# Optimization experiments

Measured on AMD Instinct MI355X. Metric: run time of the kernel, lower is better.

The kernel has to match this reference:

```python
import jax, jax.numpy as jnp
import numpy as np

WS = 8            # window size (square)
HEADS = 16
HEAD_DIM = 32
DIM = 512
NEG_INF = float('-inf')


def _create_mask(ws, disp, upper_lower, left_right):
    size = ws * ws
    m = np.zeros((size, size), dtype=np.float32)
    d = disp
    if upper_lower:
        m[-d * ws:, :-d * ws] = NEG_INF
        m[:-d * ws, -d * ws:] = NEG_INF
    if left_right:
        m = m.reshape(ws, ws, ws, ws)
        m[:, -d:, :, :-d] = NEG_INF
        m[:, :-d, :, -d:] = NEG_INF
        m = m.reshape(size, size)
    return m


def _relative_indices(ws):
    coords = np.array([[x, y] for x in range(ws) for y in range(ws)])  # [ws^2, 2]
    dist = coords[None, :, :] - coords[:, None, :]                      # [ws^2, ws^2, 2]
    dist += ws - 1
    return dist.astype(np.int64)


_REL_IDX = _relative_indices(WS)                      # [64, 64, 2]
_UL_MASK = jnp.asarray(_create_mask(WS, WS // 2, True, False))   # [64, 64]
_LR_MASK = jnp.asarray(_create_mask(WS, WS // 2, False, True))   # [64, 64]


def setup_inputs() -> dict:
    key = jax.random.key(0)
    ks = jax.random.split(key, 5)
    b, n = 16, 64
    return {
        'x': jax.random.normal(ks[0], (b, n, n, DIM), dtype=jnp.float32),
        'w_qkv': jax.random.normal(ks[1], (3 * HEADS * HEAD_DIM, DIM), dtype=jnp.float32) * 0.02,
        'pos_embedding': jax.random.normal(ks[2], (2 * WS - 1, 2 * WS - 1), dtype=jnp.float32),
        'w_out': jax.random.normal(ks[3], (DIM, HEADS * HEAD_DIM), dtype=jnp.float32) * 0.02,
        'b_out': jax.random.normal(ks[4], (DIM,), dtype=jnp.float32) * 0.02,
    }


def reference(x, w_qkv, pos_embedding, w_out, b_out):
    disp = WS // 2
    scale = HEAD_DIM ** -0.5
    b, n_h, n_w, _ = x.shape
    nw_h, nw_w = n_h // WS, n_w // WS

    # cyclic shift (shifted=True)
    x = jnp.roll(x, shift=(-disp, -disp), axis=(1, 2))

    qkv = x @ w_qkv.T                                   # [b, n_h, n_w, 3*h*d]
    qkv = qkv.reshape(b, nw_h, WS, nw_w, WS, 3, HEADS, HEAD_DIM)
    # -> [3, b, heads, n_windows, window_tokens, head_dim]
    qkv = qkv.transpose(5, 0, 6, 1, 3, 2, 4, 7).reshape(
        3, b, HEADS, nw_h * nw_w, WS * WS, HEAD_DIM)
    q, k, v = qkv[0], qkv[1], qkv[2]

    dots = jnp.einsum('bhwid,bhwjd->bhwij', q, k) * scale
    # relative position bias
    dots = dots + pos_embedding[_REL_IDX[:, :, 0], _REL_IDX[:, :, 1]]
    # shift masks: last window-row and last window-column
    dots = dots.at[:, :, -nw_w:].add(_UL_MASK)
    dots = dots.at[:, :, nw_w - 1::nw_w].add(_LR_MASK)

    attn = jax.nn.softmax(dots, axis=-1)
    out = jnp.einsum('bhwij,bhwjd->bhwid', attn, v)     # [b,h,nw,ws^2,d]

    out = out.reshape(b, HEADS, nw_h, nw_w, WS, WS, HEAD_DIM)
    out = out.transpose(0, 2, 4, 3, 5, 1, 6).reshape(b, n_h, n_w, HEADS * HEAD_DIM)
    out = out @ w_out.T + b_out

    out = jnp.roll(out, shift=(disp, disp), axis=(1, 2))
    return out
```

## Files before the change

kernel.cpp:

```cpp
#include <hip/hip_runtime.h>
#include <hip/hip_bf16.h>
#include <stdint.h>

typedef __bf16 bf16;
typedef __attribute__((ext_vector_type(4))) float f32x4;
typedef __attribute__((ext_vector_type(8))) bf16 bf16x8;
typedef __attribute__((ext_vector_type(4))) bf16 bf16x4;

#define AS1 __attribute__((address_space(1)))
#define AS3 __attribute__((address_space(3)))

static __device__ __forceinline__ void gload_lds16(const bf16* g, bf16* l) {
  __builtin_amdgcn_global_load_lds((const AS1 void*)g, (AS3 void*)l, 16, 0, 0);
}

#define BAR __builtin_amdgcn_s_barrier()
#define SCHED0 __builtin_amdgcn_sched_barrier(0)
#define VMC_(n) asm volatile("s_waitcnt vmcnt(" #n ")" ::: "memory")
#define VMC(n) VMC_(n)
#define LGKM0 asm volatile("s_waitcnt lgkmcnt(0)" ::: "memory")

#define STAGE_A(gsrc, dst, kt_) do {                                          \
  _Pragma("unroll") for (int s_ = 0; s_ < 4; ++s_) {                          \
    int idx_ = s_ * 256 + tid;                                                \
    int r_ = idx_ >> 3, c_ = idx_ & 7;                                        \
    gload_lds16((gsrc) + (size_t)r_ * 512 + ((kt_) << 6) + ((c_ ^ (r_ & 7)) << 3), \
                (dst) + idx_ * 8);                                            \
  }                                                                           \
} while (0)

#define LOADB(ktq, NCOLX) do {                                                \
  const bf16* bp_ = Bptr + (size_t)(ktq) * ((size_t)(NCOLX) * 64);            \
  _Pragma("unroll") for (int cb_ = 0; cb_ < 4; ++cb_)                         \
  _Pragma("unroll") for (int ks_ = 0; ks_ < 2; ++ks_)                         \
    bfr[cb_][ks_] = *(const bf16x8*)(bp_ + cb_ * 128 + (size_t)ks_ * (NCOLX) * 32); \
} while (0)

#define LOADB6(ktq) do {                                                      \
  const bf16* bp_ = Bptr + (size_t)(ktq) * 98304;                             \
  _Pragma("unroll") for (int cb_ = 0; cb_ < 6; ++cb_)                         \
  _Pragma("unroll") for (int ks_ = 0; ks_ < 2; ++ks_)                         \
    bfr[cb_][ks_] = *(const bf16x8*)(bp_ + cb_ * 128 + ks_ * 49152);          \
} while (0)

#define KLOOP_BD(Ag, NCOLX)                                                   \
  f32x4 acc[4][4] = {};                                                       \
  bf16x8 af[4][2], bfr[4][2];                                                 \
  STAGE_A(Ag, SA0, 0);                                                        \
  LOADB(0, NCOLX);                                                            \
  VMC(8); BAR;                                                                \
  STAGE_A(Ag, SA1, 1);                                                        \
  _Pragma("unroll 2")                                                         \
  for (int kt = 0; kt < 8; ++kt) {                                            \
    bf16* Ap = (kt & 1) ? SA1 : SA0;                                          \
    _Pragma("unroll") for (int i_ = 0; i_ < 4; ++i_) {                        \
      int ra_ = wr + i_ * 16 + lr;                                            \
      _Pragma("unroll") for (int ks_ = 0; ks_ < 2; ++ks_)                     \
        af[i_][ks_] = *(const bf16x8*)(Ap + ra_ * 64 + (((ks_ * 4 + lg) ^ (ra_ & 7)) << 3)); \
    }                                                                         \
    LGKM0; SCHED0;                                                            \
    __builtin_amdgcn_s_setprio(1);                                            \
    _Pragma("unroll") for (int i_ = 0; i_ < 4; ++i_)                          \
    _Pragma("unroll") for (int j_ = 0; j_ < 4; ++j_)                          \
    _Pragma("unroll") for (int ks_ = 0; ks_ < 2; ++ks_)                       \
      acc[i_][j_] = __builtin_amdgcn_mfma_f32_16x16x32_bf16(                  \
          af[i_][ks_], bfr[j_][ks_], acc[i_][j_], 0, 0, 0);                   \
    __builtin_amdgcn_s_setprio(0);                                            \
    if (kt < 7) LOADB(kt + 1, NCOLX);                                         \
    if (kt < 7) { VMC(8); }                                                   \
    BAR;                                                                      \
    if (kt < 6) STAGE_A(Ag, Ap, kt + 2);                                      \
  }

__global__ __launch_bounds__(256) void prep_x(const float* __restrict__ x,
                                              bf16* __restrict__ xs) {
  int m = blockIdx.x * 8 + (threadIdx.x >> 5);
  int lane = threadIdx.x & 31;
  int b = m >> 12, win = (m >> 6) & 63, t = m & 63;
  int ip = ((win >> 3) << 3) + (t >> 3);
  int jp = ((win & 7) << 3) + (t & 7);
  int io = (ip + 4) & 63, jo = (jp + 4) & 63;
  const float* src = x + ((((size_t)(b << 6) + io) << 6) + jo) * 512;
  bf16* dst = xs + ((size_t)m << 9);
  #pragma unroll
  for (int c0 = 0; c0 < 512; c0 += 128) {
    int c = c0 + lane * 4;
    float4 v = *(const float4*)(src + c);
    bf16x4 o = { (bf16)v.x, (bf16)v.y, (bf16)v.z, (bf16)v.w };
    *(bf16x4*)(dst + c) = o;
  }
}

__global__ __launch_bounds__(256) void prep_w(const float* __restrict__ wqkv,
                                              const float* __restrict__ wout,
                                              bf16* __restrict__ wqkv_bt,
                                              bf16* __restrict__ wout_bt) {
  int r = blockIdx.x * 8 + (threadIdx.x >> 5);
  int lane = threadIdx.x & 31;
  const float* src;
  bf16* dstb;
  int ncol, col;
  float sc = 1.0f;
  if (r < 1536) {
    int part = r >> 9, h = (r >> 5) & 15, d = r & 31;
    src = wqkv + (size_t)r * 512; dstb = wqkv_bt; ncol = 1536;
    col = h * 96 + part * 32 + d;
    if (part == 0) sc = 0.17677669529663689f;
  } else {
    src = wout + (size_t)(r - 1536) * 512; dstb = wout_bt; ncol = 512; col = r - 1536;
  }
  #pragma unroll
  for (int kb = lane; kb < 64; kb += 32) {
    float4 v0 = *(const float4*)(src + kb * 8);
    float4 v1 = *(const float4*)(src + kb * 8 + 4);
    bf16x8 o = { (bf16)(v0.x * sc), (bf16)(v0.y * sc), (bf16)(v0.z * sc), (bf16)(v0.w * sc),
                 (bf16)(v1.x * sc), (bf16)(v1.y * sc), (bf16)(v1.z * sc), (bf16)(v1.w * sc) };
    *(bf16x8*)(dstb + ((size_t)kb * ncol + col) * 8) = o;
  }
}

__global__ __launch_bounds__(256) void prep_bias(const float* __restrict__ pos,
                                                 float* __restrict__ bias4) {
  for (int idx = threadIdx.x; idx < 4 * 4096; idx += 256) {
    int ty = idx >> 12, ij = idx & 4095;
    int i = ij >> 6, j = ij & 63;
    int rx = ((j >> 3) - (i >> 3)) + 7;
    int ry = ((j & 7) - (i & 7)) + 7;
    float v = pos[rx * 15 + ry];
    if ((ty & 1) && (((i ^ j) >> 5) & 1)) v = -1e30f;
    if ((ty & 2) && (((i ^ j) >> 2) & 1)) v = -1e30f;
    bias4[idx] = v;
  }
}

__global__ __launch_bounds__(256, 3) void qkv_attn(
    const bf16* __restrict__ xs, const bf16* __restrict__ wb2,
    const float* __restrict__ bias4, bf16* __restrict__ ao) {
  __shared__ bf16 smb[16384];
  bf16* SA0 = smb; bf16* SA1 = smb + 8192;

  const int tid = threadIdx.x, wave = tid >> 6, lane = tid & 63;
  const int ww = wave >> 1, rh = wave & 1;
  const int lr = lane & 15, lg = lane >> 4;

  int bid = blockIdx.x;
  bid = (bid & 7) * 1024 + (bid >> 3);
  const int mt = bid >> 4, h = bid & 15;

  const bf16* Ag = xs + ((size_t)mt * 128) * 512;
  const bf16* Bptr = wb2 + (((size_t)lg * 1536) + h * 96 + lr) * 8;

  f32x4 acc[2][6] = {};
  bf16x8 af[2][2], bfr[6][2];

  STAGE_A(Ag, SA0, 0);
  LOADB6(0);
  VMC(12); BAR;
  STAGE_A(Ag, SA1, 1);
  #pragma unroll 2
  for (int kt = 0; kt < 8; ++kt) {
    bf16* Ap = (kt & 1) ? SA1 : SA0;
    #pragma unroll
    for (int i_ = 0; i_ < 2; ++i_) {
      int ra_ = ww * 64 + rh * 32 + i_ * 16 + lr;
      #pragma unroll
      for (int ks_ = 0; ks_ < 2; ++ks_)
        af[i_][ks_] = *(const bf16x8*)(Ap + ra_ * 64 + (((ks_ * 4 + lg) ^ (ra_ & 7)) << 3));
    }
    LGKM0; SCHED0;
    __builtin_amdgcn_s_setprio(1);
    #pragma unroll
    for (int i_ = 0; i_ < 2; ++i_)
      #pragma unroll
      for (int j_ = 0; j_ < 6; ++j_)
        #pragma unroll
        for (int ks_ = 0; ks_ < 2; ++ks_)
          acc[i_][j_] = __builtin_amdgcn_mfma_f32_16x16x32_bf16(
              af[i_][ks_], bfr[j_][ks_], acc[i_][j_], 0, 0, 0);
    __builtin_amdgcn_s_setprio(0);
    if (kt < 7) { LOADB6(kt + 1); VMC(12); }
    BAR;
    if (kt < 6) STAGE_A(Ag, Ap, kt + 2);
  }

  bf16* Eu = smb + ww * 6144;
  bf16* Ev = Eu + 4096;
  #pragma unroll
  for (int i = 0; i < 2; ++i)
    #pragma unroll
    for (int r = 0; r < 4; ++r) {
      int row = rh * 32 + i * 16 + (lg << 2) + r;
      #pragma unroll
      for (int j = 0; j < 4; ++j) {
        int c = j * 16 + lr;
        Eu[row * 64 + (c ^ ((row & 7) << 3))] = (bf16)acc[i][j][r];
      }
      #pragma unroll
      for (int j = 4; j < 6; ++j) {
        int cv = (j - 4) * 16 + lr;
        Ev[cv * 64 + (row ^ ((cv & 7) << 3))] = (bf16)acc[i][j][r];
      }
    }
  LGKM0; BAR;

  bf16x8 qf[2], kf[4];
  #pragma unroll
  for (int i = 0; i < 2; ++i) {
    int ra = rh * 32 + i * 16 + lr;
    qf[i] = *(const bf16x8*)(Eu + ra * 64 + ((lg << 3) ^ ((ra & 7) << 3)));
  }
  #pragma unroll
  for (int j = 0; j < 4; ++j) {
    int rb = j * 16 + lr;
    kf[j] = *(const bf16x8*)(Eu + rb * 64 + ((32 + (lg << 3)) ^ ((rb & 7) << 3)));
  }
  f32x4 s[2][4] = {};
  #pragma unroll
  for (int i = 0; i < 2; ++i)
    #pragma unroll
    for (int j = 0; j < 4; ++j)
      s[i][j] = __builtin_amdgcn_mfma_f32_16x16x32_bf16(qf[i], kf[j], s[i][j], 0, 0, 0);

  const int gw = mt * 2 + ww;
  const int win = gw & 63;
  const int ty = ((win >= 56) ? 1 : 0) | (((win & 7) == 7) ? 2 : 0);
  const float* bt = bias4 + ty * 4096;
  #pragma unroll
  for (int i = 0; i < 2; ++i)
    #pragma unroll
    for (int r = 0; r < 4; ++r) {
      int grow = rh * 32 + i * 16 + (lg << 2) + r;
      #pragma unroll
      for (int j = 0; j < 4; ++j)
        s[i][j][r] += bt[grow * 64 + j * 16 + lr];
    }
  #pragma unroll
  for (int i = 0; i < 2; ++i)
    #pragma unroll
    for (int r = 0; r < 4; ++r) {
      float mx = fmaxf(fmaxf(s[i][0][r], s[i][1][r]), fmaxf(s[i][2][r], s[i][3][r]));
      mx = fmaxf(mx, __shfl_xor(mx, 1));
      mx = fmaxf(mx, __shfl_xor(mx, 2));
      mx = fmaxf(mx, __shfl_xor(mx, 4));
      mx = fmaxf(mx, __shfl_xor(mx, 8));
      float sum = 0.f;
      #pragma unroll
      for (int j = 0; j < 4; ++j) { s[i][j][r] = __expf(s[i][j][r] - mx); sum += s[i][j][r]; }
      sum += __shfl_xor(sum, 1);
      sum += __shfl_xor(sum, 2);
      sum += __shfl_xor(sum, 4);
      sum += __shfl_xor(sum, 8);
      float inv = 1.0f / sum;
      #pragma unroll
      for (int j = 0; j < 4; ++j) s[i][j][r] *= inv;
    }
  BAR;
  #pragma unroll
  for (int i = 0; i < 2; ++i)
    #pragma unroll
    for (int r = 0; r < 4; ++r) {
      int row = rh * 32 + i * 16 + (lg << 2) + r;
      #pragma unroll
      for (int j = 0; j < 4; ++j) {
        int c = j * 16 + lr;
        Eu[row * 64 + (c ^ ((row & 7) << 3))] = (bf16)s[i][j][r];
      }
    }
  LGKM0; SCHED0;
  bf16x8 vf[2][2];
  #pragma unroll
  for (int kk = 0; kk < 2; ++kk)
    #pragma unroll
    for (int nj = 0; nj < 2; ++nj) {
      int dv = nj * 16 + lr;
      vf[kk][nj] = *(const bf16x8*)(Ev + dv * 64 + ((kk * 32 + (lg << 3)) ^ ((dv & 7) << 3)));
    }
  f32x4 o[2][2] = {};
  #pragma unroll
  for (int kk = 0; kk < 2; ++kk)
    #pragma unroll
    for (int mi = 0; mi < 2; ++mi) {
      int ra = rh * 32 + mi * 16 + lr;
      bf16x8 pa = *(const bf16x8*)(Eu + ra * 64 + ((kk * 32 + (lg << 3)) ^ ((ra & 7) << 3)));
      #pragma unroll
      for (int nj = 0; nj < 2; ++nj)
        o[mi][nj] = __builtin_amdgcn_mfma_f32_16x16x32_bf16(pa, vf[kk][nj], o[mi][nj], 0, 0, 0);
    }
  bf16* dst = ao + ((size_t)(mt * 128 + ww * 64)) * 512 + h * 32;
  #pragma unroll
  for (int mi = 0; mi < 2; ++mi)
    #pragma unroll
    for (int r = 0; r < 4; ++r) {
      int t = rh * 32 + mi * 16 + (lg << 2) + r;
      #pragma unroll
      for (int nj = 0; nj < 2; ++nj)
        dst[(size_t)t * 512 + nj * 16 + lr] = (bf16)o[mi][nj][r];
    }
}

__global__ __launch_bounds__(256, 3) void gemm_out(
    const bf16* __restrict__ ao, const bf16* __restrict__ wob,
    const float* __restrict__ bout, float* __restrict__ out) {
  __shared__ bf16 SA[2][8192];
  bf16* SA0 = SA[0]; bf16* SA1 = SA[1];

  const int tid = threadIdx.x, wave = tid >> 6, lane = tid & 63;
  int bid = blockIdx.x;
  bid = (bid & 7) * 256 + (bid >> 3);
  const int mt = bid >> 2, nt = bid & 3;
  const bf16* Ag = ao + ((size_t)mt * 128) * 512;
  const int wr = (wave >> 1) << 6, wc = (wave & 1) << 6;
  const int lr = lane & 15, lg = lane >> 4;
  const bf16* Bptr = wob + (((size_t)lg * 512) + nt * 128 + wc + lr) * 8;

  KLOOP_BD(Ag, 512)

  float bv[4];
  #pragma unroll
  for (int j = 0; j < 4; ++j) bv[j] = bout[nt * 128 + wc + j * 16 + lr];
  #pragma unroll
  for (int i = 0; i < 4; ++i)
    #pragma unroll
    for (int r = 0; r < 4; ++r) {
      int m = (mt << 7) + wr + i * 16 + (lg << 2) + r;
      int b = m >> 12, win = (m >> 6) & 63, t = m & 63;
      int ip = ((win >> 3) << 3) + (t >> 3);
      int jp = ((win & 7) << 3) + (t & 7);
      int io = (ip + 4) & 63, jo = (jp + 4) & 63;
      float* orow = out + ((((size_t)(b << 6) + io) << 6) + jo) * 512 + nt * 128 + wc;
      #pragma unroll
      for (int j = 0; j < 4; ++j)
        orow[j * 16 + lr] = acc[i][j][r] + bv[j];
    }
}

extern "C" void kernel_launch(void* const* d_in, const int* in_sizes, int n_in,
                              void* d_out, int out_size, void* d_ws, size_t ws_size,
                              hipStream_t stream) {
  const float* x    = (const float*)d_in[0];
  const float* wqkv = (const float*)d_in[1];
  const float* pos  = (const float*)d_in[2];
  const float* wout = (const float*)d_in[3];
  const float* bout = (const float*)d_in[4];
  float* out = (float*)d_out;

  char* ws = (char*)d_ws;
  bf16* xs      = (bf16*)(ws);
  bf16* ao      = (bf16*)(ws + 67108864);
  bf16* wqkv_bt = (bf16*)(ws + 268435456);
  bf16* wout_bt = (bf16*)(ws + 270008320);
  float* bias4  = (float*)(ws + 270532608);

  prep_x<<<dim3(8192), dim3(256), 0, stream>>>(x, xs);
  prep_w<<<dim3(256), dim3(256), 0, stream>>>(wqkv, wout, wqkv_bt, wout_bt);
  prep_bias<<<dim3(1), dim3(256), 0, stream>>>(pos, bias4);
  qkv_attn<<<dim3(8192), dim3(256), 0, stream>>>(xs, wqkv_bt, bias4, ao);
  gemm_out<<<dim3(2048), dim3(256), 0, stream>>>(ao, wout_bt, bout, out);
}
```

Before: 275.3 us.

## Store x in k-blocked layout and load A fragments directly from global memory

prep_x now writes the shifted bf16 activations in a k-block-major layout (8 bf16 per row per k-block), one thread per token. qkv_attn then reads A fragments straight into registers from global memory instead of staging through LDS with barriers. The k-loop is fully unrolled with double-buffered A and split B register sets so loads overlap MFMAs. This drops LDS staging and barriers and shrinks shared memory. In exchange, prep_x gets poorly coalesced strided writes and only 256 blocks, and the A reads are less efficient 16-byte gathers.

```diff
diff --git a/kernel.cpp b/kernel.cpp
--- a/kernel.cpp
+++ b/kernel.cpp
@@ -34,13 +34,6 @@
   _Pragma("unroll") for (int cb_ = 0; cb_ < 4; ++cb_)                         \
   _Pragma("unroll") for (int ks_ = 0; ks_ < 2; ++ks_)                         \
     bfr[cb_][ks_] = *(const bf16x8*)(bp_ + cb_ * 128 + (size_t)ks_ * (NCOLX) * 32); \
-} while (0)
-
-#define LOADB6(ktq) do {                                                      \
-  const bf16* bp_ = Bptr + (size_t)(ktq) * 98304;                             \
-  _Pragma("unroll") for (int cb_ = 0; cb_ < 6; ++cb_)                         \
-  _Pragma("unroll") for (int ks_ = 0; ks_ < 2; ++ks_)                         \
-    bfr[cb_][ks_] = *(const bf16x8*)(bp_ + cb_ * 128 + ks_ * 49152);          \
 } while (0)
 
 #define KLOOP_BD(Ag, NCOLX)                                                   \
@@ -73,21 +66,21 @@
   }
 
 __global__ __launch_bounds__(256) void prep_x(const float* __restrict__ x,
-                                              bf16* __restrict__ xs) {
-  int m = blockIdx.x * 8 + (threadIdx.x >> 5);
-  int lane = threadIdx.x & 31;
+                                              bf16* __restrict__ xst) {
+  int m = blockIdx.x * 256 + threadIdx.x;
   int b = m >> 12, win = (m >> 6) & 63, t = m & 63;
   int ip = ((win >> 3) << 3) + (t >> 3);
   int jp = ((win & 7) << 3) + (t & 7);
   int io = (ip + 4) & 63, jo = (jp + 4) & 63;
   const float* src = x + ((((size_t)(b << 6) + io) << 6) + jo) * 512;
-  bf16* dst = xs + ((size_t)m << 9);
-  #pragma unroll
-  for (int c0 = 0; c0 < 512; c0 += 128) {
-    int c = c0 + lane * 4;
-    float4 v = *(const float4*)(src + c);
-    bf16x4 o = { (bf16)v.x, (bf16)v.y, (bf16)v.z, (bf16)v.w };
-    *(bf16x4*)(dst + c) = o;
+  bf16* dst = xst + (size_t)m * 8;
+  #pragma unroll 4
+  for (int kb = 0; kb < 64; ++kb) {
+    float4 v0 = *(const float4*)(src + kb * 8);
+    float4 v1 = *(const float4*)(src + kb * 8 + 4);
+    bf16x8 o = { (bf16)v0.x, (bf16)v0.y, (bf16)v0.z, (bf16)v0.w,
+                 (bf16)v1.x, (bf16)v1.y, (bf16)v1.z, (bf16)v1.w };
+    *(bf16x8*)(dst + (size_t)kb * 524288) = o;
   }
 }
 
@@ -133,11 +126,41 @@
   }
 }
 
+#define LOADAF(dst, ktq) do {                                                 \
+  _Pragma("unroll") for (int i_ = 0; i_ < 2; ++i_)                            \
+  _Pragma("unroll") for (int ks_ = 0; ks_ < 2; ++ks_)                         \
+    dst[i_][ks_] = *(const bf16x8*)(Aptr + ((size_t)((ktq) * 8 + ks_ * 4 + lg)) * 524288 + i_ * 128); \
+} while (0)
+
+#define LOADB_H(set, ktq, hf) do {                                            \
+  const bf16* bp_ = Bptr + (size_t)(ktq) * 98304 + (hf) * 384;                \
+  _Pragma("unroll") for (int cb_ = 0; cb_ < 3; ++cb_)                         \
+  _Pragma("unroll") for (int ks_ = 0; ks_ < 2; ++ks_)                         \
+    set[cb_][ks_] = *(const bf16x8*)(bp_ + cb_ * 128 + ks_ * 49152);          \
+} while (0)
+
+#define MM3(afs, bs, j0)                                                      \
+  _Pragma("unroll") for (int i_ = 0; i_ < 2; ++i_)                            \
+  _Pragma("unroll") for (int jj_ = 0; jj_ < 3; ++jj_)                         \
+  _Pragma("unroll") for (int ks_ = 0; ks_ < 2; ++ks_)                         \
+    acc[i_][(j0) + jj_] = __builtin_amdgcn_mfma_f32_16x16x32_bf16(            \
+        afs[i_][ks_], bs[jj_][ks_], acc[i_][(j0) + jj_], 0, 0, 0);
+
+#define KTS(CUR, NXT, KT_, V2) do {                                           \
+  VMC(6); SCHED0;                                                             \
+  __builtin_amdgcn_s_setprio(1); MM3(CUR, bfrX, 0);                           \
+  __builtin_amdgcn_s_setprio(0);                                              \
+  if ((KT_) < 7) { LOADAF(NXT, (KT_) + 1); LOADB_H(bfrX, (KT_) + 1, 0); }     \
+  VMC(V2); SCHED0;                                                            \
+  __builtin_amdgcn_s_setprio(1); MM3(CUR, bfrY, 3);                           \
+  __builtin_amdgcn_s_setprio(0);                                              \
+  if ((KT_) < 7) LOADB_H(bfrY, (KT_) + 1, 1);                                 \
+} while (0)
+
 __global__ __launch_bounds__(256, 3) void qkv_attn(
-    const bf16* __restrict__ xs, const bf16* __restrict__ wb2,
+    const bf16* __restrict__ xst, const bf16* __restrict__ wb2,
     const float* __restrict__ bias4, bf16* __restrict__ ao) {
-  __shared__ bf16 smb[16384];
-  bf16* SA0 = smb; bf16* SA1 = smb + 8192;
+  __shared__ bf16 smb[12288];
 
   const int tid = threadIdx.x, wave = tid >> 6, lane = tid & 63;
   const int ww = wave >> 1, rh = wave & 1;
@@ -147,41 +170,21 @@
   bid = (bid & 7) * 1024 + (bid >> 3);
   const int mt = bid >> 4, h = bid & 15;
 
-  const bf16* Ag = xs + ((size_t)mt * 128) * 512;
+  const bf16* Aptr = xst + ((size_t)(mt * 128 + ww * 64 + rh * 32 + lr)) * 8;
   const bf16* Bptr = wb2 + (((size_t)lg * 1536) + h * 96 + lr) * 8;
 
   f32x4 acc[2][6] = {};
-  bf16x8 af[2][2], bfr[6][2];
-
-  STAGE_A(Ag, SA0, 0);
-  LOADB6(0);
-  VMC(12); BAR;
-  STAGE_A(Ag, SA1, 1);
-  #pragma unroll 2
-  for (int kt = 0; kt < 8; ++kt) {
-    bf16* Ap = (kt & 1) ? SA1 : SA0;
-    #pragma unroll
-    for (int i_ = 0; i_ < 2; ++i_) {
-      int ra_ = ww * 64 + rh * 32 + i_ * 16 + lr;
-      #pragma unroll
-      for (int ks_ = 0; ks_ < 2; ++ks_)
-        af[i_][ks_] = *(const bf16x8*)(Ap + ra_ * 64 + (((ks_ * 4 + lg) ^ (ra_ & 7)) << 3));
-    }
-    LGKM0; SCHED0;
-    __builtin_amdgcn_s_setprio(1);
-    #pragma unroll
-    for (int i_ = 0; i_ < 2; ++i_)
-      #pragma unroll
-      for (int j_ = 0; j_ < 6; ++j_)
-        #pragma unroll
-        for (int ks_ = 0; ks_ < 2; ++ks_)
-          acc[i_][j_] = __builtin_amdgcn_mfma_f32_16x16x32_bf16(
-              af[i_][ks_], bfr[j_][ks_], acc[i_][j_], 0, 0, 0);
-    __builtin_amdgcn_s_setprio(0);
-    if (kt < 7) { LOADB6(kt + 1); VMC(12); }
-    BAR;
-    if (kt < 6) STAGE_A(Ag, Ap, kt + 2);
-  }
+  bf16x8 afA[2][2], afB[2][2], bfrX[3][2], bfrY[3][2];
+
+  LOADAF(afA, 0); LOADB_H(bfrX, 0, 0); LOADB_H(bfrY, 0, 1);
+  KTS(afA, afB, 0, 10);
+  KTS(afB, afA, 1, 10);
+  KTS(afA, afB, 2, 10);
+  KTS(afB, afA, 3, 10);
+  KTS(afA, afB, 4, 10);
+  KTS(afB, afA, 5, 10);
+  KTS(afA, afB, 6, 10);
+  KTS(afB, afA, 7, 0);
 
   bf16* Eu = smb + ww * 6144;
   bf16* Ev = Eu + 4096;
@@ -345,15 +348,15 @@
   float* out = (float*)d_out;
 
   char* ws = (char*)d_ws;
-  bf16* xs      = (bf16*)(ws);
+  bf16* xst     = (bf16*)(ws);
   bf16* ao      = (bf16*)(ws + 67108864);
   bf16* wqkv_bt = (bf16*)(ws + 268435456);
   bf16* wout_bt = (bf16*)(ws + 270008320);
   float* bias4  = (float*)(ws + 270532608);
 
-  prep_x<<<dim3(8192), dim3(256), 0, stream>>>(x, xs);
+  prep_x<<<dim3(256), dim3(256), 0, stream>>>(x, xst);
   prep_w<<<dim3(256), dim3(256), 0, stream>>>(wqkv, wout, wqkv_bt, wout_bt);
   prep_bias<<<dim3(1), dim3(256), 0, stream>>>(pos, bias4);
-  qkv_attn<<<dim3(8192), dim3(256), 0, stream>>>(xs, wqkv_bt, bias4, ao);
+  qkv_attn<<<dim3(8192), dim3(256), 0, stream>>>(xst, wqkv_bt, bias4, ao);
   gemm_out<<<dim3(2048), dim3(256), 0, stream>>>(ao, wout_bt, bout, out);
 }
```

Result: faster. 264.1 us (-4.1%).
